# Optimization experiments

Measured on AMD Instinct MI355X. Metric: run time of the kernel, lower is better.

Reference implementation:

```python
import jax, jax.numpy as jnp
import numpy as np

N, T, C = 4, 2048, 1024
H = 16
D = C // H  # head_dim = 64


def setup_inputs() -> dict:
    key = jax.random.key(0)
    ks = jax.random.split(key, 6)
    s = 1.0 / np.sqrt(C)
    return {
        "x": jax.random.normal(ks[0], (N, T, C), dtype=jnp.float32),
        "Wq": jax.random.normal(ks[1], (C, C), dtype=jnp.float32) * s,
        "Wk": jax.random.normal(ks[2], (C, C), dtype=jnp.float32) * s,
        "Wv": jax.random.normal(ks[3], (C, C), dtype=jnp.float32) * s,
        "Wo": jax.random.normal(ks[4], (C, C), dtype=jnp.float32) * s,
        "bo": jax.random.normal(ks[5], (C,), dtype=jnp.float32) * s,
    }


def reference(x, Wq, Wk, Wv, Wo, bo):
    n, t, c = x.shape
    # torch nn.Linear: y = x @ W.T
    q = (x @ Wq.T).reshape(n, t, H, D).transpose(0, 2, 1, 3)  # [N,H,T,D]
    k = (x @ Wk.T).reshape(n, t, H, D).transpose(0, 2, 1, 3)
    v = (x @ Wv.T).reshape(n, t, H, D).transpose(0, 2, 1, 3)
    # NOTE: module scales by sqrt(embed_dim), not sqrt(head_dim)
    energy = jnp.einsum("nhqd,nhkd->nhqk", q, k) / jnp.sqrt(jnp.float32(c))
    causal = jnp.tril(jnp.ones((t, t), dtype=bool))  # [T,T]
    energy = jnp.where(causal[None, None], energy, -jnp.inf)
    attn = jax.nn.softmax(energy, axis=-1)
    out = jnp.einsum("nhqk,nhkd->nhqd", attn, v)  # [N,H,T,D]
    out = out.transpose(0, 2, 1, 3).reshape(n, t, c)
    return out @ Wo.T + bo
```

## Files before the change

### kernel.cpp

```cpp
#include <hip/hip_runtime.h>
#include <math.h>

#define N_ 4
#define T_ 2048
#define C_ 1024
#define H_ 16
#define D_ 64
#define NTC (N_*T_*C_)
#define WELEM (C_*C_)

typedef float f32x4  __attribute__((ext_vector_type(4)));
typedef float f32x16 __attribute__((ext_vector_type(16)));
typedef short bf16x8 __attribute__((ext_vector_type(8)));

static __device__ __forceinline__ unsigned short f2bf(float f) {
    union { float f; unsigned u; } v; v.f = f;
    unsigned r = v.u + 0x7FFFu + ((v.u >> 16) & 1u);
    return (unsigned short)(r >> 16);
}

static __device__ __forceinline__ unsigned cvtpk(float lo, float hi) {
    unsigned r;
    asm("v_cvt_pk_bf16_f32 %0, %1, %2" : "=v"(r) : "v"(lo), "v"(hi));
    return r;
}
#define PLSWAP(a, b) asm("v_permlane32_swap_b32 %0, %1" : "+v"(a), "+v"(b))

#define GLDS16(gptr, lptr) \
    __builtin_amdgcn_global_load_lds((const __attribute__((address_space(1))) void*)(gptr), \
                                     (__attribute__((address_space(3))) void*)(lptr), 16, 0, 0)

__global__ __launch_bounds__(256) void cast_x(const float* __restrict__ src,
                                              unsigned short* __restrict__ dst) {
    const int i = blockIdx.x * 256 + threadIdx.x;
    const float4 a = ((const float4*)src)[i * 2];
    const float4 b = ((const float4*)src)[i * 2 + 1];
    unsigned short u[8] = {f2bf(a.x), f2bf(a.y), f2bf(a.z), f2bf(a.w),
                           f2bf(b.x), f2bf(b.y), f2bf(b.z), f2bf(b.w)};
    *(uint4*)&dst[(size_t)i * 8] = *(const uint4*)u;
}

__global__ __launch_bounds__(256) void cast_w4(const float* __restrict__ w0,
                                               const float* __restrict__ w1,
                                               const float* __restrict__ w2,
                                               const float* __restrict__ w3,
                                               unsigned short* __restrict__ dst) {
    const int z = blockIdx.y;
    const float* __restrict__ src = (z == 0) ? w0 : (z == 1) ? w1 : (z == 2) ? w2 : w3;
    unsigned short* __restrict__ d = dst + (size_t)z * WELEM;
    const int i = blockIdx.x * 256 + threadIdx.x;
    const float4 a = ((const float4*)src)[i * 2];
    const float4 b = ((const float4*)src)[i * 2 + 1];
    unsigned short u[8] = {f2bf(a.x), f2bf(a.y), f2bf(a.z), f2bf(a.w),
                           f2bf(b.x), f2bf(b.y), f2bf(b.z), f2bf(b.w)};
    *(uint4*)&d[(size_t)i * 8] = *(const uint4*)u;
}

#define GEMM_BODY(Aptr, Bptr)                                                           \
    __shared__ __align__(16) unsigned short Abuf[128 * 32];                             \
    __shared__ __align__(16) unsigned short Bbuf[128 * 32];                             \
    const int tid  = threadIdx.x;                                                       \
    const int lane = tid & 63;                                                          \
    const int w    = tid >> 6;                                                          \
    const int lo   = lane & 15;                                                         \
    const int hi   = lane >> 4;                                                         \
    const int wm   = w >> 1;                                                            \
    const int wn   = w & 1;                                                             \
    const int rowBase = blockIdx.x * 128;                                               \
    const int colBase = blockIdx.y * 128;                                               \
    f32x4 acc[4][4];                                                                    \
    _Pragma("unroll")                                                                   \
    for (int i = 0; i < 4; ++i)                                                         \
        _Pragma("unroll")                                                               \
        for (int j = 0; j < 4; ++j) acc[i][j] = (f32x4)(0.f);                           \
    const int i0 = tid, i1 = tid + 256;                                                 \
    const int r0 = i0 >> 2, s0_ = i0 & 3, g0 = s0_ ^ ((r0 >> 1) & 3);                   \
    const int r1 = i1 >> 2, s1_ = i1 & 3, g1 = s1_ ^ ((r1 >> 1) & 3);                   \
    const unsigned short* gA0 = (Aptr) + (size_t)(rowBase + r0) * C_ + g0 * 8;          \
    const unsigned short* gA1 = (Aptr) + (size_t)(rowBase + r1) * C_ + g1 * 8;          \
    const unsigned short* gB0 = (Bptr) + (size_t)(colBase + r0) * C_ + g0 * 8;          \
    const unsigned short* gB1 = (Bptr) + (size_t)(colBase + r1) * C_ + g1 * 8;          \
    for (int k0 = 0; k0 < C_; k0 += 32) {                                               \
        GLDS16(gA0 + k0, &Abuf[i0 * 8]);                                                \
        GLDS16(gA1 + k0, &Abuf[i1 * 8]);                                                \
        GLDS16(gB0 + k0, &Bbuf[i0 * 8]);                                                \
        GLDS16(gB1 + k0, &Bbuf[i1 * 8]);                                                \
        __syncthreads();                                                                \
        bf16x8 af[4], bfv[4];                                                           \
        _Pragma("unroll")                                                               \
        for (int mi = 0; mi < 4; ++mi) {                                                \
            const int row = wm * 64 + mi * 16 + lo;                                     \
            const int slot = hi ^ ((row >> 1) & 3);                                     \
            af[mi] = *(const bf16x8*)&Abuf[row * 32 + slot * 8];                        \
        }                                                                               \
        _Pragma("unroll")                                                               \
        for (int ni = 0; ni < 4; ++ni) {                                                \
            const int row = wn * 64 + ni * 16 + lo;                                     \
            const int slot = hi ^ ((row >> 1) & 3);                                     \
            bfv[ni] = *(const bf16x8*)&Bbuf[row * 32 + slot * 8];                       \
        }                                                                               \
        _Pragma("unroll")                                                               \
        for (int mi = 0; mi < 4; ++mi)                                                  \
            _Pragma("unroll")                                                           \
            for (int ni = 0; ni < 4; ++ni)                                              \
                acc[mi][ni] = __builtin_amdgcn_mfma_f32_16x16x32_bf16(af[mi], bfv[ni],  \
                                                                     acc[mi][ni], 0, 0, 0); \
        __syncthreads();                                                                \
    }

__global__ __launch_bounds__(256) void qkv_fused(const unsigned short* __restrict__ A,
                                                 const unsigned short* __restrict__ Wall,
                                                 unsigned short* __restrict__ qkvout) {
    const int z = blockIdx.z;
    const unsigned short* __restrict__ B = Wall + (size_t)z * WELEM;
    unsigned short* __restrict__ Y = qkvout + (size_t)z * NTC;
    const float oscale = (z == 0) ? (0.03125f * 1.44269504f) : 1.0f;

    GEMM_BODY(A, B)

    if (z < 2) {
        #pragma unroll
        for (int mi = 0; mi < 4; ++mi) {
            #pragma unroll
            for (int r = 0; r < 4; ++r) {
                const int row = rowBase + wm * 64 + mi * 16 + hi * 4 + r;
                const int nn = row >> 11, tt = row & (T_ - 1);
                #pragma unroll
                for (int ni = 0; ni < 4; ++ni) {
                    const int col = colBase + wn * 64 + ni * 16 + lo;
                    Y[((size_t)((nn * H_ + (col >> 6)) * T_ + tt)) * D_ + (col & 63)] =
                        f2bf(acc[mi][ni][r] * oscale);
                }
            }
        }
    } else {
        #pragma unroll
        for (int mi = 0; mi < 4; ++mi) {
            #pragma unroll
            for (int r = 0; r < 4; ++r) {
                const int row = rowBase + wm * 64 + mi * 16 + hi * 4 + r;
                const int nn = row >> 11, tt = row & (T_ - 1);
                #pragma unroll
                for (int ni = 0; ni < 4; ++ni) {
                    const int col = colBase + wn * 64 + ni * 16 + lo;
                    Y[(size_t)((nn * 16 + (col >> 6)) * 64 + (col & 63)) * T_ + tt] =
                        f2bf(acc[mi][ni][r]);
                }
            }
        }
    }
}

__global__ __launch_bounds__(256) void out_gemm(const unsigned short* __restrict__ A,
                                                const unsigned short* __restrict__ B,
                                                const float* __restrict__ bo,
                                                float* __restrict__ out) {
    GEMM_BODY(A, B)

    float bias[4];
    #pragma unroll
    for (int ni = 0; ni < 4; ++ni) bias[ni] = bo[colBase + wn * 64 + ni * 16 + lo];
    #pragma unroll
    for (int mi = 0; mi < 4; ++mi) {
        #pragma unroll
        for (int r = 0; r < 4; ++r) {
            const int row = rowBase + wm * 64 + mi * 16 + hi * 4 + r;
            #pragma unroll
            for (int ni = 0; ni < 4; ++ni) {
                const int col = colBase + wn * 64 + ni * 16 + lo;
                out[(size_t)row * C_ + col] = acc[mi][ni][r] + bias[ni];
            }
        }
    }
}

__global__ __launch_bounds__(256, 4) void attn_mfma(const unsigned short* __restrict__ qg,
                                                    const unsigned short* __restrict__ kg,
                                                    const unsigned short* __restrict__ vtg,
                                                    unsigned short* __restrict__ ob) {
    __shared__ __align__(16) unsigned short Kt[2][64 * 64];
    __shared__ __align__(16) unsigned short Vt[2][64 * 64];

    const int tid  = threadIdx.x;
    const int w    = tid >> 6;
    const int lane = tid & 63;
    const int ql   = lane & 31;
    const int h    = lane >> 5;
    const int bid  = blockIdx.x;
    const int g    = bid >> 6;
    const int gi   = g & 3;
    const int gq   = g >> 2;
    const int qtile = (gq == 0) ? (15 - gi) : (gq == 1) ? (8 + gi) : (gq == 2) ? (7 - gi) : gi;
    const int nh   = bid & 63;
    const int qb   = qtile * 128;
    const size_t base  = (size_t)nh * (T_ * D_);
    const size_t vbase = (size_t)nh * 64 * T_;
    const int qrow0 = qb + w * 32;

    bf16x8 qf[4];
    #pragma unroll
    for (int dsl = 0; dsl < 4; ++dsl)
        qf[dsl] = *(const bf16x8*)(qg + base + (size_t)(qrow0 + ql) * D_ + dsl * 16 + h * 8);

    f32x16 acc0 = (f32x16)(0.f), acc1 = (f32x16)(0.f);
    float mrun = -INFINITY, lrun = 0.f;

    const int mynkt  = (qrow0 >> 6) + 1;
    const int nktmax = (qb >> 6) + 2;
    const int csubdiag = (w & 1) + 1;

    const int i0 = tid, i1 = tid + 256;
    const int kr0 = i0 >> 3, kc0 = ((i0 & 7) ^ (kr0 & 7)) * 8;
    const int kr1 = i1 >> 3, kc1 = ((i1 & 7) ^ (kr1 & 7)) * 8;

    #define STAGE(kt_, buf_)                                                            \
        do {                                                                            \
            const int kb_ = (kt_) * 64;                                                 \
            GLDS16(kg + base + (size_t)(kb_ + kr0) * D_ + kc0, &Kt[buf_][i0 * 8]);      \
            GLDS16(kg + base + (size_t)(kb_ + kr1) * D_ + kc1, &Kt[buf_][i1 * 8]);      \
            GLDS16(vtg + vbase + (size_t)kr0 * T_ + kb_ + kc0, &Vt[buf_][i0 * 8]);      \
            GLDS16(vtg + vbase + (size_t)kr1 * T_ + kb_ + kc1, &Vt[buf_][i1 * 8]);      \
        } while (0)

    STAGE(0, 0);
    __syncthreads();
    int cur = 0;

    for (int kt = 0; kt < nktmax; ++kt) {
        if (kt + 1 < nktmax) STAGE(kt + 1, cur ^ 1);

        if (kt < mynkt) {
            const bool diag = (kt == mynkt - 1);
            const int csub = diag ? csubdiag : 2;
            const unsigned short* Kb = Kt[cur];
            const unsigned short* Vb = Vt[cur];

            f32x16 s0, s1;
            __builtin_amdgcn_s_setprio(1);
            {
                f32x16 z = (f32x16)(0.f);
                #pragma unroll
                for (int dsl = 0; dsl < 4; ++dsl) {
                    const bf16x8 ka = *(const bf16x8*)&Kb[ql * 64 + ((dsl * 2 + h) ^ (ql & 7)) * 8];
                    z = __builtin_amdgcn_mfma_f32_32x32x16_bf16(ka, qf[dsl], z, 0, 0, 0);
                }
                s0 = z;
            }
            if (csub > 1) {
                f32x16 z = (f32x16)(0.f);
                #pragma unroll
                for (int dsl = 0; dsl < 4; ++dsl) {
                    const bf16x8 ka = *(const bf16x8*)&Kb[(32 + ql) * 64 + ((dsl * 2 + h) ^ (ql & 7)) * 8];
                    z = __builtin_amdgcn_mfma_f32_32x32x16_bf16(ka, qf[dsl], z, 0, 0, 0);
                }
                s1 = z;
            }
            __builtin_amdgcn_s_setprio(0);

            if (diag) {
                #pragma unroll
                for (int r = 0; r < 16; ++r) {
                    const int rc = (r & 3) + 8 * (r >> 2) + 4 * h;
                    if (csub == 1) { if (rc > ql) s0[r] = -1e30f; }
                    else           { if (rc > ql) s1[r] = -1e30f; }
                }
            }

            float tm;
            {
                float t[8];
                if (csub > 1) {
                    #pragma unroll
                    for (int r = 0; r < 8; ++r)
                        t[r] = fmaxf(fmaxf(s0[2 * r], s0[2 * r + 1]),
                                     fmaxf(s1[2 * r], s1[2 * r + 1]));
                } else {
                    #pragma unroll
                    for (int r = 0; r < 8; ++r) t[r] = fmaxf(s0[2 * r], s0[2 * r + 1]);
                }
                t[0] = fmaxf(t[0], t[4]); t[1] = fmaxf(t[1], t[5]);
                t[2] = fmaxf(t[2], t[6]); t[3] = fmaxf(t[3], t[7]);
                t[0] = fmaxf(t[0], t[2]); t[1] = fmaxf(t[1], t[3]);
                tm = fmaxf(t[0], t[1]);
                tm = fmaxf(tm, __shfl_xor(tm, 32));
            }

            if (!__all(tm <= mrun + 8.f)) {
                const float mnew = fmaxf(mrun, tm);
                const float fsc = exp2f(mrun - mnew);
                mrun = mnew;
                lrun *= fsc;
                #pragma unroll
                for (int r = 0; r < 16; ++r) {
                    const float f = __shfl(fsc, (r & 3) + 8 * (r >> 2) + 4 * h);
                    acc0[r] *= f; acc1[r] *= f;
                }
            }

            #pragma unroll
            for (int r = 0; r < 16; ++r) s0[r] = exp2f(s0[r] - mrun);
            if (csub > 1) {
                #pragma unroll
                for (int r = 0; r < 16; ++r) s1[r] = exp2f(s1[r] - mrun);
            }
            {
                float t[8];
                if (csub > 1) {
                    #pragma unroll
                    for (int r = 0; r < 8; ++r)
                        t[r] = (s0[2 * r] + s0[2 * r + 1]) + (s1[2 * r] + s1[2 * r + 1]);
                } else {
                    #pragma unroll
                    for (int r = 0; r < 8; ++r) t[r] = s0[2 * r] + s0[2 * r + 1];
                }
                t[0] += t[4]; t[1] += t[5]; t[2] += t[6]; t[3] += t[7];
                t[0] += t[2]; t[1] += t[3];
                float psum = t[0] + t[1];
                psum += __shfl_xor(psum, 32);
                lrun += psum;
            }

            bf16x8 pa[4];
            #pragma unroll
            for (int a = 0; a < 2; ++a) {
                if (a < csub) {
                    #pragma unroll
                    for (int b = 0; b < 2; ++b) {
                        const f32x16& P = a ? s1 : s0;
                        unsigned w0 = cvtpk(P[8 * b + 0], P[8 * b + 1]);
                        unsigned w1 = cvtpk(P[8 * b + 2], P[8 * b + 3]);
                        unsigned w2 = cvtpk(P[8 * b + 4], P[8 * b + 5]);
                        unsigned w3 = cvtpk(P[8 * b + 6], P[8 * b + 7]);
                        PLSWAP(w0, w2);
                        PLSWAP(w1, w3);
                        unsigned wd[4] = {w0, w1, w2, w3};
                        pa[2 * a + b] = *(bf16x8*)wd;
                    }
                }
            }

            __builtin_amdgcn_s_setprio(1);
            #pragma unroll
            for (int ks = 0; ks < 4; ++ks) {
                if (ks < 2 * csub) {
                    const bf16x8 vf0 = *(const bf16x8*)&Vb[ql * 64 + ((ks * 2 + h) ^ (ql & 7)) * 8];
                    const bf16x8 vf1 = *(const bf16x8*)&Vb[(32 + ql) * 64 + ((ks * 2 + h) ^ (ql & 7)) * 8];
                    acc0 = __builtin_amdgcn_mfma_f32_32x32x16_bf16(pa[ks], vf0, acc0, 0, 0, 0);
                    acc1 = __builtin_amdgcn_mfma_f32_32x32x16_bf16(pa[ks], vf1, acc1, 0, 0, 0);
                }
            }
            __builtin_amdgcn_s_setprio(0);
        }
        __syncthreads();
        cur ^= 1;
    }

    const float linv = 1.f / lrun;
    const int nn = nh >> 4, hh = nh & 15;
    #pragma unroll
    for (int r = 0; r < 16; ++r) {
        const int rc = (r & 3) + 8 * (r >> 2) + 4 * h;
        const float li = __shfl(linv, rc);
        const size_t rb = (size_t)(nn * T_ + qrow0 + rc) * C_ + hh * 64;
        ob[rb + ql]      = f2bf(acc0[r] * li);
        ob[rb + 32 + ql] = f2bf(acc1[r] * li);
    }
    #undef STAGE
}

extern "C" void kernel_launch(void* const* d_in, const int* in_sizes, int n_in,
                              void* d_out, int out_size, void* d_ws, size_t ws_size,
                              hipStream_t stream) {
    const float* x  = (const float*)d_in[0];
    const float* Wq = (const float*)d_in[1];
    const float* Wk = (const float*)d_in[2];
    const float* Wv = (const float*)d_in[3];
    const float* Wo = (const float*)d_in[4];
    const float* bo = (const float*)d_in[5];
    float* out = (float*)d_out;

    unsigned short* ws = (unsigned short*)d_ws;
    unsigned short* x_bf   = ws;
    unsigned short* w_bf   = x_bf + (size_t)NTC;
    unsigned short* qkv_bf = w_bf + (size_t)4 * WELEM;
    unsigned short* a_bf   = qkv_bf + (size_t)3 * NTC;

    cast_x<<<NTC / (8 * 256), 256, 0, stream>>>(x, x_bf);
    dim3 gw(WELEM / (8 * 256), 4);
    cast_w4<<<gw, 256, 0, stream>>>(Wq, Wk, Wv, Wo, w_bf);

    dim3 gq(N_ * T_ / 128, C_ / 128, 3);
    qkv_fused<<<gq, 256, 0, stream>>>(x_bf, w_bf, qkv_bf);

    attn_mfma<<<(T_ / 128) * (N_ * H_), 256, 0, stream>>>(
        qkv_bf, qkv_bf + (size_t)NTC, qkv_bf + (size_t)2 * NTC, a_bf);

    dim3 gg(N_ * T_ / 128, C_ / 128);
    out_gemm<<<gg, 256, 0, stream>>>(a_bf, w_bf + 3 * (size_t)WELEM, bo, out);
}
```

Measured before the change: 197.9 us.

## Merge cast kernels, relax attention launch bounds, use simple descending tile order

Merges the x and weight bf16 cast kernels into one launch that picks its source by flat element index, so one kernel launch is saved. Changes the attention kernel's launch bounds from 4 to 2 blocks per SM, which gives the compiler more registers per thread but may lower occupancy. Replaces the interleaved query-tile schedule with a plain longest-first descending order, which changes how causal work is balanced across CUs.

New measurement: 178.6 us. 1.11x faster.

```diff
diff --git a/kernel.cpp b/kernel.cpp
--- a/kernel.cpp
+++ b/kernel.cpp
@@ -30,30 +30,29 @@
     __builtin_amdgcn_global_load_lds((const __attribute__((address_space(1))) void*)(gptr), \
                                      (__attribute__((address_space(3))) void*)(lptr), 16, 0, 0)
 
-__global__ __launch_bounds__(256) void cast_x(const float* __restrict__ src,
-                                              unsigned short* __restrict__ dst) {
+__global__ __launch_bounds__(256) void cast_all(const float* __restrict__ x,
+                                                const float* __restrict__ w0,
+                                                const float* __restrict__ w1,
+                                                const float* __restrict__ w2,
+                                                const float* __restrict__ w3,
+                                                unsigned short* __restrict__ dst) {
     const int i = blockIdx.x * 256 + threadIdx.x;
-    const float4 a = ((const float4*)src)[i * 2];
-    const float4 b = ((const float4*)src)[i * 2 + 1];
+    const size_t e = (size_t)i * 8;
+    const float* __restrict__ src;
+    size_t soff;
+    if (e < (size_t)NTC) {
+        src = x; soff = e;
+    } else {
+        const size_t e2 = e - (size_t)NTC;
+        const int z = (int)(e2 >> 20);
+        src = (z == 0) ? w0 : (z == 1) ? w1 : (z == 2) ? w2 : w3;
+        soff = e2 & (WELEM - 1);
+    }
+    const float4 a = *(const float4*)(src + soff);
+    const float4 b = *(const float4*)(src + soff + 4);
     unsigned short u[8] = {f2bf(a.x), f2bf(a.y), f2bf(a.z), f2bf(a.w),
                            f2bf(b.x), f2bf(b.y), f2bf(b.z), f2bf(b.w)};
-    *(uint4*)&dst[(size_t)i * 8] = *(const uint4*)u;
-}
-
-__global__ __launch_bounds__(256) void cast_w4(const float* __restrict__ w0,
-                                               const float* __restrict__ w1,
-                                               const float* __restrict__ w2,
-                                               const float* __restrict__ w3,
-                                               unsigned short* __restrict__ dst) {
-    const int z = blockIdx.y;
-    const float* __restrict__ src = (z == 0) ? w0 : (z == 1) ? w1 : (z == 2) ? w2 : w3;
-    unsigned short* __restrict__ d = dst + (size_t)z * WELEM;
-    const int i = blockIdx.x * 256 + threadIdx.x;
-    const float4 a = ((const float4*)src)[i * 2];
-    const float4 b = ((const float4*)src)[i * 2 + 1];
-    unsigned short u[8] = {f2bf(a.x), f2bf(a.y), f2bf(a.z), f2bf(a.w),
-                           f2bf(b.x), f2bf(b.y), f2bf(b.z), f2bf(b.w)};
-    *(uint4*)&d[(size_t)i * 8] = *(const uint4*)u;
+    *(uint4*)&dst[e] = *(const uint4*)u;
 }
 
 #define GEMM_BODY(Aptr, Bptr)                                                           \
@@ -174,7 +173,7 @@
     }
 }
 
-__global__ __launch_bounds__(256, 4) void attn_mfma(const unsigned short* __restrict__ qg,
+__global__ __launch_bounds__(256, 2) void attn_mfma(const unsigned short* __restrict__ qg,
                                                     const unsigned short* __restrict__ kg,
                                                     const unsigned short* __restrict__ vtg,
                                                     unsigned short* __restrict__ ob) {
@@ -187,10 +186,7 @@
     const int ql   = lane & 31;
     const int h    = lane >> 5;
     const int bid  = blockIdx.x;
-    const int g    = bid >> 6;
-    const int gi   = g & 3;
-    const int gq   = g >> 2;
-    const int qtile = (gq == 0) ? (15 - gi) : (gq == 1) ? (8 + gi) : (gq == 2) ? (7 - gi) : gi;
+    const int qtile = 15 - (bid >> 6);
     const int nh   = bid & 63;
     const int qb   = qtile * 128;
     const size_t base  = (size_t)nh * (T_ * D_);
@@ -385,9 +381,7 @@
     unsigned short* qkv_bf = w_bf + (size_t)4 * WELEM;
     unsigned short* a_bf   = qkv_bf + (size_t)3 * NTC;
 
-    cast_x<<<NTC / (8 * 256), 256, 0, stream>>>(x, x_bf);
-    dim3 gw(WELEM / (8 * 256), 4);
-    cast_w4<<<gw, 256, 0, stream>>>(Wq, Wk, Wv, Wo, w_bf);
+    cast_all<<<(NTC + 4 * WELEM) / (8 * 256), 256, 0, stream>>>(x, Wq, Wk, Wv, Wo, x_bf);
 
     dim3 gq(N_ * T_ / 128, C_ / 128, 3);
     qkv_fused<<<gq, 256, 0, stream>>>(x_bf, w_bf, qkv_bf);
```
